# Kernel optimization log

Hardware: AMD Instinct MI355X
Metric: run time of the kernel (lower is better)

## Reference

```python
import jax, jax.numpy as jnp
import numpy as np

EPS = 1e-6


def _rmsnorm(x, w):
    var = jnp.mean(x * x, axis=-1, keepdims=True)
    return x * jax.lax.rsqrt(var + EPS) * w


def _rotate_half(x):
    h = x.shape[-1] // 2
    return jnp.concatenate([-x[..., h:], x[..., :h]], axis=-1)


def setup_inputs() -> dict:
    key = jax.random.key(0)
    B, T, H = 2, 2048, 2048
    nh, nkv, d = 16, 8, 128
    max_pos = 4096
    ks = jax.random.split(key, 6)
    s = 0.02
    x = jax.random.normal(ks[0], (B, T, H), jnp.float32)
    # real RoPE tables (Qwen3 uses rope_theta=1e6)
    inv_freq = 1.0 / (1e6 ** (np.arange(0, d, 2, dtype=np.float64) / d))
    freqs = np.outer(np.arange(max_pos), inv_freq)
    emb = np.concatenate([freqs, freqs], axis=-1)
    cos = jnp.asarray(np.cos(emb), jnp.float32)
    sin = jnp.asarray(np.sin(emb), jnp.float32)
    position_ids = jnp.broadcast_to(jnp.arange(T, dtype=jnp.int32)[None, :], (B, T))
    Wq = jax.random.normal(ks[1], (nh * d, H), jnp.float32) * s
    Wk = jax.random.normal(ks[2], (nkv * d, H), jnp.float32) * s
    Wv = jax.random.normal(ks[3], (nkv * d, H), jnp.float32) * s
    Wo = jax.random.normal(ks[4], (H, nh * d), jnp.float32) * s
    q_norm_w = jnp.ones((d,), jnp.float32)
    k_norm_w = jnp.ones((d,), jnp.float32)
    return {"x": x, "cos": cos, "sin": sin, "position_ids": position_ids,
            "Wq": Wq, "Wk": Wk, "Wv": Wv, "Wo": Wo,
            "q_norm_w": q_norm_w, "k_norm_w": k_norm_w}


def reference(x, cos, sin, position_ids, Wq, Wk, Wv, Wo, q_norm_w, k_norm_w):
    B, T, H = x.shape
    d = q_norm_w.shape[0]
    nh = Wq.shape[0] // d
    nkv = Wk.shape[0] // d
    groups = nh // nkv

    # QKV projections (F.linear: x @ W.T)
    q = jnp.einsum('bth,oh->bto', x, Wq).reshape(B, T, nh, d).transpose(0, 2, 1, 3)   # [B,nh,T,d]
    k = jnp.einsum('bth,oh->bto', x, Wk).reshape(B, T, nkv, d).transpose(0, 2, 1, 3)  # [B,nkv,T,d]
    v = jnp.einsum('bth,oh->bto', x, Wv).reshape(B, T, nkv, d).transpose(0, 2, 1, 3)

    # per-head RMSNorm on q and k
    q = _rmsnorm(q, q_norm_w)
    k = _rmsnorm(k, k_norm_w)

    # RoPE
    cos_b = cos[position_ids][:, None, :, :]  # [B,1,T,d]
    sin_b = sin[position_ids][:, None, :, :]
    q = q * cos_b + _rotate_half(q) * sin_b
    k = k * cos_b + _rotate_half(k) * sin_b

    # GQA expand (repeat_interleave along head dim)
    if groups > 1:
        k = jnp.repeat(k, groups, axis=1)
        v = jnp.repeat(v, groups, axis=1)

    # causal SDPA
    scale = 1.0 / jnp.sqrt(jnp.asarray(d, x.dtype))
    scores = jnp.einsum('bhqd,bhkd->bhqk', q, k) * scale  # [B,nh,T,T]
    causal = jnp.tril(jnp.ones((T, T), bool))
    scores = jnp.where(causal[None, None], scores, jnp.asarray(-jnp.inf, scores.dtype))
    probs = jax.nn.softmax(scores, axis=-1)
    attn = jnp.einsum('bhqk,bhkd->bhqd', probs, v)  # [B,nh,T,d]

    attn = attn.transpose(0, 2, 1, 3).reshape(B, T, nh * d)
    return jnp.einsum('bto,ho->bth', attn, Wo)
```

## Files before the change

### kernel.cpp

```cpp
#include <hip/hip_runtime.h>
#include <stdint.h>
#include <stddef.h>

typedef unsigned short u16;
typedef __attribute__((ext_vector_type(4))) unsigned short u16x4;
typedef __attribute__((ext_vector_type(8))) short bf16x8;
typedef __attribute__((ext_vector_type(4))) float f32x4;
typedef __attribute__((ext_vector_type(16))) float f32x16;

#define B_   2
#define T_   2048
#define NH   16
#define NKV  8
#define HD   128

#define QSCALE 0.1275174457f

__device__ __forceinline__ u16 f2bf(float f) {
  union { float f; uint32_t u; } v; v.f = f;
  uint32_t u = v.u;
  u += 0x7FFFu + ((u >> 16) & 1u);
  return (u16)(u >> 16);
}
__device__ __forceinline__ float bf2f(u16 h) {
  union { uint32_t u; float f; } v; v.u = ((uint32_t)h) << 16;
  return v.f;
}
__device__ __forceinline__ uint32_t cvt_pk_bf16(float lo, float hi) {
  uint32_t r;
  asm("v_cvt_pk_bf16_f32 %0, %1, %2" : "=v"(r) : "v"(lo), "v"(hi));
  return r;
}
__device__ __forceinline__ float fexp2(float x) {
  float r;
  asm("v_exp_f32 %0, %1" : "=v"(r) : "v"(x));
  return r;
}

__device__ __forceinline__ void gload_lds16(const void* g, void* l) {
  __builtin_amdgcn_global_load_lds(
      (__attribute__((address_space(1))) void*)g,
      (__attribute__((address_space(3))) void*)l, 16, 0, 0);
}

__global__ __launch_bounds__(256) void cvt_all(const float* __restrict__ x,
                                               const float* __restrict__ Wq,
                                               const float* __restrict__ Wk,
                                               const float* __restrict__ Wv,
                                               const float* __restrict__ Wo,
                                               u16* __restrict__ ws0) {
  const int blk = blockIdx.x;
  const float* src; u16* dst; int lb;
  if (blk < 8192)       { src = x;  dst = ws0;              lb = blk; }
  else if (blk < 12288) { src = Wq; dst = ws0 +  8388608;   lb = blk - 8192; }
  else if (blk < 14336) { src = Wk; dst = ws0 + 12582912;   lb = blk - 12288; }
  else if (blk < 16384) { src = Wv; dst = ws0 + 14680064;   lb = blk - 14336; }
  else                  { src = Wo; dst = ws0 + 16777216;   lb = blk - 16384; }
  const int i = lb * 256 + threadIdx.x;
  float4 v = reinterpret_cast<const float4*>(src)[i];
  u16x4 o;
  o.x = f2bf(v.x); o.y = f2bf(v.y); o.z = f2bf(v.z); o.w = f2bf(v.w);
  reinterpret_cast<u16x4*>(dst)[i] = o;
}

template<int BM, int BN, int STORE>
__global__ __launch_bounds__(512, 2) void gemm2(const u16* __restrict__ A,
                                                const u16* __restrict__ Bm,
                                                void* __restrict__ C0,
                                                void* __restrict__ C1,
                                                void* __restrict__ C2,
                                                int M, int N, int K) {
  constexpr int FM  = BM / 32;
  constexpr int FN  = BN / 64;
  constexpr int ASZ = BM * 64;
  constexpr int BSZ = BN * 64;
  __shared__ u16 lds[2 * (ASZ + BSZ)];

  const int tid  = threadIdx.x;
  const int lane = tid & 63;
  const int wid  = tid >> 6;
  const int lr   = lane & 15;
  const int lg   = lane >> 4;
  const int wm0 = (wid >> 2) * (BM / 2);
  const int wn0 = (wid & 3) * (BN / 4);

  const int s  = ((blockIdx.x & 7) << 5) | (blockIdx.x >> 3);
  const int nx = N / BN;
  const int m0 = (s / nx) * BM;
  const int n0 = (s % nx) * BN;

  f32x4 acc[FM][FN];
#pragma unroll
  for (int i = 0; i < FM; ++i)
#pragma unroll
    for (int j = 0; j < FN; ++j) acc[i][j] = (f32x4){0.f, 0.f, 0.f, 0.f};

  auto stage = [&](int kt, int p) {
    const int k0 = kt << 6;
    u16* Ab = lds + p * (ASZ + BSZ);
    u16* Bb = Ab + ASZ;
#pragma unroll
    for (int it = 0; it < BM / 64; ++it) {
      const int CI = it * 512 + tid;
      const int row = CI >> 3, c = CI & 7;
      gload_lds16(A + (size_t)(m0 + row) * K + k0 + ((c ^ (row & 7)) << 3),
                  (char*)Ab + (size_t)CI * 16);
    }
#pragma unroll
    for (int it = 0; it < BN / 64; ++it) {
      const int CI = it * 512 + tid;
      const int row = CI >> 3, c = CI & 7;
      gload_lds16(Bm + (size_t)(n0 + row) * K + k0 + ((c ^ (row & 7)) << 3),
                  (char*)Bb + (size_t)CI * 16);
    }
  };

  const int nk = K >> 6;
  stage(0, 0);
  __syncthreads();
  int cur = 0;
  for (int kt = 0; kt < nk; ++kt) {
    if (kt + 1 < nk) stage(kt + 1, cur ^ 1);
    const u16* Ab = lds + cur * (ASZ + BSZ);
    const u16* Bb = Ab + ASZ;
#pragma unroll
    for (int kk = 0; kk < 2; ++kk) {
      bf16x8 af[FM], bfr[FN];
#pragma unroll
      for (int mt = 0; mt < FM; ++mt) {
        const int ar = wm0 + mt * 16 + lr;
        af[mt] = *reinterpret_cast<const bf16x8*>(
            (const char*)Ab + ar * 128 + ((kk * 64 + lg * 16) ^ ((ar & 7) << 4)));
      }
#pragma unroll
      for (int nt = 0; nt < FN; ++nt) {
        const int br = wn0 + nt * 16 + lr;
        bfr[nt] = *reinterpret_cast<const bf16x8*>(
            (const char*)Bb + br * 128 + ((kk * 64 + lg * 16) ^ ((br & 7) << 4)));
      }
      __builtin_amdgcn_s_setprio(1);
#pragma unroll
      for (int mt = 0; mt < FM; ++mt)
#pragma unroll
        for (int nt = 0; nt < FN; ++nt)
          acc[mt][nt] = __builtin_amdgcn_mfma_f32_16x16x32_bf16(
              af[mt], bfr[nt], acc[mt][nt], 0, 0, 0);
      __builtin_amdgcn_s_setprio(0);
    }
    __syncthreads();
    cur ^= 1;
  }

  if (STORE == 3) {
    u16* Qd = (u16*)C0; u16* Kd = (u16*)C1; u16* Vd = (u16*)C2;
    if (n0 < 2048) {
#pragma unroll
      for (int mt = 0; mt < FM; ++mt) {
        const int row = m0 + wm0 + mt * 16 + lg * 4;
#pragma unroll
        for (int nt = 0; nt < FN; ++nt) {
          const int col = n0 + wn0 + nt * 16 + lr;
#pragma unroll
          for (int r = 0; r < 4; ++r)
            Qd[(size_t)(row + r) * 2048 + col] = f2bf(acc[mt][nt][r]);
        }
      }
    } else if (n0 < 3072) {
#pragma unroll
      for (int mt = 0; mt < FM; ++mt) {
        const int row = m0 + wm0 + mt * 16 + lg * 4;
#pragma unroll
        for (int nt = 0; nt < FN; ++nt) {
          const int col = n0 + wn0 + nt * 16 + lr - 2048;
#pragma unroll
          for (int r = 0; r < 4; ++r)
            Kd[(size_t)(row + r) * 1024 + col] = f2bf(acc[mt][nt][r]);
        }
      }
    } else {
#pragma unroll
      for (int mt = 0; mt < FM; ++mt) {
        const int row = m0 + wm0 + mt * 16 + lg * 4;
        const int b = row >> 11;
        const int t = row & (T_ - 1);
#pragma unroll
        for (int nt = 0; nt < FN; ++nt) {
          const int vc = n0 + wn0 + nt * 16 + lr - 3072;
          u16x4 v;
          v.x = f2bf(acc[mt][nt][0]); v.y = f2bf(acc[mt][nt][1]);
          v.z = f2bf(acc[mt][nt][2]); v.w = f2bf(acc[mt][nt][3]);
          *reinterpret_cast<u16x4*>(Vd + ((size_t)(b * 1024 + vc)) * T_ + t) = v;
        }
      }
    }
  } else {
    float* C = (float*)C0;
#pragma unroll
    for (int mt = 0; mt < FM; ++mt) {
      const int row = m0 + wm0 + mt * 16 + lg * 4;
#pragma unroll
      for (int nt = 0; nt < FN; ++nt) {
        const int col = n0 + wn0 + nt * 16 + lr;
#pragma unroll
        for (int r = 0; r < 4; ++r)
          C[(size_t)(row + r) * N + col] = acc[mt][nt][r];
      }
    }
  }
}

__global__ __launch_bounds__(256) void rms_rope(u16* __restrict__ Q, u16* __restrict__ Kb,
                                                const float* __restrict__ cosT,
                                                const float* __restrict__ sinT,
                                                const int* __restrict__ pos,
                                                const float* __restrict__ qw,
                                                const float* __restrict__ kw) {
  const int wave = blockIdx.x * 4 + (threadIdx.x >> 6);
  const int lane = threadIdx.x & 63;
  const int bt = wave & (B_ * T_ - 1);
  const int hh = wave >> 12;
  u16* ptr;
  const float* w;
  float post;
  if (hh < NH) { ptr = Q + (size_t)bt * (NH * HD) + hh * HD; w = qw; post = QSCALE; }
  else         { ptr = Kb + (size_t)bt * (NKV * HD) + (hh - NH) * HD; w = kw; post = 1.0f; }
  const int p = pos[bt];

  float e0 = bf2f(ptr[lane]);
  float e1 = bf2f(ptr[lane + 64]);
  float ss = e0 * e0 + e1 * e1;
#pragma unroll
  for (int off = 1; off < 64; off <<= 1) ss += __shfl_xor(ss, off, 64);
  const float r = rsqrtf(ss * (1.0f / 128.0f) + 1e-6f) * post;
  const float n0 = e0 * r * w[lane];
  const float n1 = e1 * r * w[lane + 64];
  const float c0 = cosT[(size_t)p * HD + lane], c1 = cosT[(size_t)p * HD + lane + 64];
  const float s0 = sinT[(size_t)p * HD + lane], s1 = sinT[(size_t)p * HD + lane + 64];
  ptr[lane]      = f2bf(n0 * c0 - n1 * s0);
  ptr[lane + 64] = f2bf(n1 * c1 + n0 * s1);
}

__global__ __launch_bounds__(256, 2) void flash_attn5(const u16* __restrict__ Qw,
                                                      const u16* __restrict__ Kw,
                                                      const u16* __restrict__ VTw,
                                                      u16* __restrict__ Ow) {
  __shared__ __align__(16) char smem[65536];

  const int tid  = threadIdx.x;
  const int lane = tid & 63;
  const int wid  = tid >> 6;
  const int rl   = lane & 31;
  const int hi   = lane >> 5;
  const int blk  = blockIdx.x;
  const int qtr = blk >> 5;
  const int qt  = (blk < 256) ? (15 - qtr) : (qtr - 8);
  const int bh  = blk & 31;
  const int b   = bh >> 4, h = bh & 15, kvh = h >> 1;
  const int q0w = qt * 128 + wid * 32;
  const int qg  = q0w + rl;
  const int kswz = (rl & 15) << 4;
  const int vswz = (rl & 7) << 4;

  bf16x8 qf[8];
  {
    const u16* qp = Qw + ((size_t)(b * T_) + qg) * (NH * HD) + h * HD + hi * 8;
#pragma unroll
    for (int kd = 0; kd < 8; ++kd) qf[kd] = *reinterpret_cast<const bf16x8*>(qp + kd * 16);
  }

  f32x16 ot[4];
#pragma unroll
  for (int dt = 0; dt < 4; ++dt)
#pragma unroll
    for (int r = 0; r < 16; ++r) ot[dt][r] = 0.f;
  float m = -1e30f, lsum = 0.f;

  auto stageKV = [&](int kt, int p) {
    char* Kb = smem + p * 32768;
    char* Vb = Kb + 16384;
    {
      const int row = tid >> 4, ch = tid & 15;
#pragma unroll
      for (int it = 0; it < 4; ++it) {
        const int rr = it * 16 + row;
        const int scol = ((ch * 16) ^ ((rr & 15) << 4)) >> 1;
        gload_lds16(Kw + ((size_t)(b * T_) + kt * 64 + rr) * (NKV * HD) + kvh * HD + scol,
                    Kb + (it * 256 + tid) * 16);
      }
    }
    {
      const int row = tid >> 3, ch = tid & 7;
#pragma unroll
      for (int it = 0; it < 4; ++it) {
        const int rr = it * 32 + row;
        const int scol = ((ch * 16) ^ ((rr & 7) << 4)) >> 1;
        gload_lds16(VTw + ((size_t)((b * NKV + kvh) * HD) + rr) * T_ + kt * 64 + scol,
                    Vb + (it * 256 + tid) * 16);
      }
    }
  };

  const int nkt = 2 * qt + 2;
  stageKV(0, 0);
  __syncthreads();
  for (int kt = 0; kt < nkt; ++kt) {
    const int cur = kt & 1;
    if (kt + 1 < nkt) stageKV(kt + 1, cur ^ 1);

    if (64 * kt <= q0w + 31) {
      const u16* Kb = (const u16*)(smem + cur * 32768);
      const u16* Vb = (const u16*)(smem + cur * 32768 + 16384);

      f32x16 s0, s1;
#pragma unroll
      for (int r = 0; r < 16; ++r) { s0[r] = 0.f; s1[r] = 0.f; }
      __builtin_amdgcn_s_setprio(1);
#pragma unroll
      for (int kd = 0; kd < 8; ++kd) {
        const int cb = (kd * 32 + hi * 16) ^ kswz;
        const bf16x8 k0 = *reinterpret_cast<const bf16x8*>((const char*)Kb + rl * 256 + cb);
        const bf16x8 k1 = *reinterpret_cast<const bf16x8*>((const char*)Kb + (32 + rl) * 256 + cb);
        s0 = __builtin_amdgcn_mfma_f32_32x32x16_bf16(k0, qf[kd], s0, 0, 0, 0);
        s1 = __builtin_amdgcn_mfma_f32_32x32x16_bf16(k1, qf[kd], s1, 0, 0, 0);
      }
      __builtin_amdgcn_s_setprio(0);

      const int kv0 = kt * 64;
      const bool maskT = (kv0 + 63 > q0w);
      float rm = -1e30f;
      if (maskT) {
#pragma unroll
        for (int r = 0; r < 16; ++r) {
          const int cr = (r & 3) + 8 * (r >> 2) + 4 * hi;
          float a = s0[r], c = s1[r];
          if (kv0 + cr > qg)      a = -1e30f;
          if (kv0 + 32 + cr > qg) c = -1e30f;
          s0[r] = a; s1[r] = c;
          rm = fmaxf(rm, fmaxf(a, c));
        }
      } else {
#pragma unroll
        for (int r = 0; r < 16; ++r) rm = fmaxf(rm, fmaxf(s0[r], s1[r]));
      }
      rm = fmaxf(rm, __shfl_xor(rm, 32));

      if (!__all(rm <= m + 8.0f)) {
        const float mn = fmaxf(m, rm);
        const float al = fexp2(m - mn);
        lsum *= al;
#pragma unroll
        for (int dt = 0; dt < 4; ++dt)
#pragma unroll
          for (int r = 0; r < 16; ++r) ot[dt][r] *= al;
        m = mn;
      }
      float rs = 0.f;
#pragma unroll
      for (int r = 0; r < 16; ++r) {
        const float p0 = fexp2(s0[r] - m);
        const float p1 = fexp2(s1[r] - m);
        s0[r] = p0; s1[r] = p1;
        rs += p0 + p1;
      }
      rs += __shfl_xor(rs, 32);
      lsum += rs;

      bf16x8 pf[2][2];
#pragma unroll
      for (int ks = 0; ks < 2; ++ks) {
        {
          uint32_t X0 = cvt_pk_bf16(s0[8 * ks + 0], s0[8 * ks + 1]);
          uint32_t X1 = cvt_pk_bf16(s0[8 * ks + 2], s0[8 * ks + 3]);
          uint32_t Y0 = cvt_pk_bf16(s0[8 * ks + 4], s0[8 * ks + 5]);
          uint32_t Y1 = cvt_pk_bf16(s0[8 * ks + 6], s0[8 * ks + 7]);
          asm volatile("v_permlane32_swap_b32 %0, %1" : "+v"(X0), "+v"(Y0));
          asm volatile("v_permlane32_swap_b32 %0, %1" : "+v"(X1), "+v"(Y1));
          union { uint32_t w[4]; bf16x8 v; } u;
          u.w[0] = X0; u.w[1] = X1; u.w[2] = Y0; u.w[3] = Y1;
          pf[0][ks] = u.v;
        }
        {
          uint32_t X0 = cvt_pk_bf16(s1[8 * ks + 0], s1[8 * ks + 1]);
          uint32_t X1 = cvt_pk_bf16(s1[8 * ks + 2], s1[8 * ks + 3]);
          uint32_t Y0 = cvt_pk_bf16(s1[8 * ks + 4], s1[8 * ks + 5]);
          uint32_t Y1 = cvt_pk_bf16(s1[8 * ks + 6], s1[8 * ks + 7]);
          asm volatile("v_permlane32_swap_b32 %0, %1" : "+v"(X0), "+v"(Y0));
          asm volatile("v_permlane32_swap_b32 %0, %1" : "+v"(X1), "+v"(Y1));
          union { uint32_t w[4]; bf16x8 v; } u;
          u.w[0] = X0; u.w[1] = X1; u.w[2] = Y0; u.w[3] = Y1;
          pf[1][ks] = u.v;
        }
      }

      __builtin_amdgcn_s_setprio(1);
#pragma unroll
      for (int dt = 0; dt < 4; ++dt) {
        const int rv = dt * 32 + rl;
#pragma unroll
        for (int kvc = 0; kvc < 2; ++kvc)
#pragma unroll
          for (int ks = 0; ks < 2; ++ks) {
            const int cb = (kvc * 64 + ks * 32 + hi * 16) ^ ((rv & 7) << 4);
            const bf16x8 vf = *reinterpret_cast<const bf16x8*>((const char*)Vb + rv * 128 + cb);
            ot[dt] = __builtin_amdgcn_mfma_f32_32x32x16_bf16(vf, pf[kvc][ks], ot[dt], 0, 0, 0);
          }
      }
      __builtin_amdgcn_s_setprio(0);
    }
    __syncthreads();
  }

  const float inv = 1.0f / lsum;
  u16* ep = (u16*)smem + wid * (32 * 136);
#pragma unroll
  for (int dt = 0; dt < 4; ++dt)
#pragma unroll
    for (int r = 0; r < 16; ++r) {
      const int d = dt * 32 + (r & 3) + 8 * (r >> 2) + 4 * hi;
      ep[rl * 136 + d] = f2bf(ot[dt][r] * inv);
    }
  const int dh = hi * 64;
  const u16* srcp = (u16*)smem + wid * (32 * 136) + rl * 136 + dh;
  u16* gdst = Ow + ((size_t)(b * T_) + q0w + rl) * (NH * HD) + h * HD + dh;
#pragma unroll
  for (int c2 = 0; c2 < 8; ++c2)
    *reinterpret_cast<bf16x8*>(gdst + c2 * 8) =
        *reinterpret_cast<const bf16x8*>(srcp + c2 * 8);
}

extern "C" void kernel_launch(void* const* d_in, const int* in_sizes, int n_in,
                              void* d_out, int out_size, void* d_ws, size_t ws_size,
                              hipStream_t stream) {
  (void)in_sizes; (void)n_in; (void)out_size; (void)ws_size;
  const float* x    = (const float*)d_in[0];
  const float* cosT = (const float*)d_in[1];
  const float* sinT = (const float*)d_in[2];
  const int*   pos  = (const int*)d_in[3];
  const float* Wq   = (const float*)d_in[4];
  const float* Wk   = (const float*)d_in[5];
  const float* Wv   = (const float*)d_in[6];
  const float* Wo   = (const float*)d_in[7];
  const float* qw   = (const float*)d_in[8];
  const float* kw   = (const float*)d_in[9];
  float* out = (float*)d_out;

  char* ws = (char*)d_ws;
  u16* xb   = (u16*)(ws + 0);
  u16* Wqb  = (u16*)(ws + 16777216);
  u16* Wob  = (u16*)(ws + 33554432);
  u16* Qws  = (u16*)(ws + 41943040);
  u16* Kws  = (u16*)(ws + 58720256);
  u16* VTws = (u16*)(ws + 67108864);
  u16* Aws  = (u16*)(ws + 75497472);

  cvt_all<<<20480, 256, 0, stream>>>(x, Wq, Wk, Wv, Wo, (u16*)ws);

  gemm2<256, 256, 3><<<256, 512, 0, stream>>>(xb, Wqb, Qws, Kws, VTws,
                                              4096, 4096, 2048);

  rms_rope<<<24576, 256, 0, stream>>>(Qws, Kws, cosT, sinT, pos, qw, kw);

  flash_attn5<<<512, 256, 0, stream>>>(Qws, Kws, VTws, Aws);

  gemm2<128, 256, 2><<<256, 512, 0, stream>>>(Aws, Wob, out, nullptr, nullptr,
                                              4096, 2048, 2048);
}
```

Before: 191.5 us.

## Add finely pipelined QKV GEMM kernel with interleaved half-tile staging

Adds a dedicated 256x256 QKV projection GEMM that splits each K-step into four MFMA phases. Each phase issues half-tile global-to-LDS loads for upcoming steps, with explicit vmcnt waits and barriers, so loads overlap compute more finely than the old double-buffered loop. It also uses a block-index swizzle for tile scheduling. The cost is more barriers and hand-tuned wait counts, which are fragile if the load counts change.

```diff
diff --git a/kernel.cpp b/kernel.cpp
--- a/kernel.cpp
+++ b/kernel.cpp
@@ -42,6 +42,11 @@
       (__attribute__((address_space(1))) void*)g,
       (__attribute__((address_space(3))) void*)l, 16, 0, 0);
 }
+
+#define WAITVM(N) do { asm volatile("s_waitcnt vmcnt(" #N ")" ::: "memory"); \
+                       __builtin_amdgcn_sched_barrier(0); } while (0)
+#define BAR()     do { __builtin_amdgcn_s_barrier(); \
+                       __builtin_amdgcn_sched_barrier(0); } while (0)
 
 __global__ __launch_bounds__(256) void cvt_all(const float* __restrict__ x,
                                                const float* __restrict__ Wq,
@@ -63,6 +68,195 @@
   reinterpret_cast<u16x4*>(dst)[i] = o;
 }
 
+__global__ __launch_bounds__(512, 2) void gemm3(const u16* __restrict__ A,
+                                                const u16* __restrict__ Bm,
+                                                void* __restrict__ C0,
+                                                void* __restrict__ C1,
+                                                void* __restrict__ C2,
+                                                int M, int N, int K) {
+  constexpr int BM = 256, BN = 256;
+  constexpr int ASZ = BM * 64;
+  constexpr int BSZ = BN * 64;
+  constexpr int RSZ = ASZ + BSZ;
+  __shared__ u16 lds[2 * RSZ];
+
+  const int tid  = threadIdx.x;
+  const int lane = tid & 63;
+  const int wid  = tid >> 6;
+  const int lr   = lane & 15;
+  const int lg   = lane >> 4;
+  const int wm0 = (wid >> 2) * 128;
+  const int wn0 = (wid & 3) * 64;
+
+  const int s  = ((blockIdx.x & 7) << 5) | (blockIdx.x >> 3);
+  const int nx = N / BN;
+  const int m0 = (s / nx) * BM;
+  const int n0 = (s % nx) * BN;
+
+  f32x4 acc[8][4];
+#pragma unroll
+  for (int i = 0; i < 8; ++i)
+#pragma unroll
+    for (int j = 0; j < 4; ++j) acc[i][j] = (f32x4){0.f, 0.f, 0.f, 0.f};
+
+  auto stageA = [&](int kt, int xh) {
+    u16* Ab = lds + (kt & 1) * RSZ;
+    const int k0 = kt << 6;
+#pragma unroll
+    for (int j = 0; j < 2; ++j) {
+      const int rowblk = j * 128 + xh * 64;
+      const int row = rowblk + (tid >> 3), c = tid & 7;
+      gload_lds16(A + (size_t)(m0 + row) * K + k0 + ((c ^ (row & 7)) << 3),
+                  (char*)Ab + ((size_t)rowblk * 8 + tid) * 16);
+    }
+  };
+  auto stageB = [&](int kt, int nh) {
+    u16* Bb = lds + (kt & 1) * RSZ + ASZ;
+    const int k0 = kt << 6;
+#pragma unroll
+    for (int j = 0; j < 2; ++j) {
+      const int blk2 = j * 2 + (tid >> 8);
+      const int row = blk2 * 64 + nh * 32 + ((tid & 255) >> 3);
+      const int c = tid & 7;
+      gload_lds16(Bm + (size_t)(n0 + row) * K + k0 + ((c ^ (row & 7)) << 3),
+                  (char*)Bb + ((size_t)row * 8 + c) * 16);
+    }
+  };
+
+  const int nk = K >> 6;
+
+  stageA(0, 0); stageB(0, 0); stageA(0, 1); stageB(0, 1);
+  stageA(1, 0); stageB(1, 0);
+  WAITVM(8);
+  BAR();
+
+  bf16x8 af[4][2], bf[2][2];
+
+#define LOAD_A(Ab, mh)                                                        \
+  _Pragma("unroll")                                                           \
+  for (int mt2 = 0; mt2 < 4; ++mt2)                                           \
+    _Pragma("unroll")                                                         \
+    for (int kk = 0; kk < 2; ++kk) {                                          \
+      const int ar = wm0 + ((mh) * 4 + mt2) * 16 + lr;                        \
+      af[mt2][kk] = *reinterpret_cast<const bf16x8*>(                         \
+          (const char*)(Ab) + ar * 128 + ((kk * 64 + lg * 16) ^ ((ar & 7) << 4))); \
+    }
+#define LOAD_B(Bb, nh)                                                        \
+  _Pragma("unroll")                                                           \
+  for (int nt2 = 0; nt2 < 2; ++nt2)                                           \
+    _Pragma("unroll")                                                         \
+    for (int kk = 0; kk < 2; ++kk) {                                          \
+      const int br = wn0 + ((nh) * 2 + nt2) * 16 + lr;                        \
+      bf[nt2][kk] = *reinterpret_cast<const bf16x8*>(                         \
+          (const char*)(Bb) + br * 128 + ((kk * 64 + lg * 16) ^ ((br & 7) << 4))); \
+    }
+#define MFMA_PHASE(mh, nh)                                                    \
+  __builtin_amdgcn_s_setprio(1);                                              \
+  _Pragma("unroll")                                                           \
+  for (int mt2 = 0; mt2 < 4; ++mt2)                                           \
+    _Pragma("unroll")                                                         \
+    for (int nt2 = 0; nt2 < 2; ++nt2)                                         \
+      _Pragma("unroll")                                                       \
+      for (int kk = 0; kk < 2; ++kk)                                          \
+        acc[(mh) * 4 + mt2][(nh) * 2 + nt2] =                                 \
+            __builtin_amdgcn_mfma_f32_16x16x32_bf16(                          \
+                af[mt2][kk], bf[nt2][kk], acc[(mh) * 4 + mt2][(nh) * 2 + nt2],\
+                0, 0, 0);                                                     \
+  __builtin_amdgcn_s_setprio(0);
+
+  for (int t = 0; t <= nk - 3; ++t) {
+    const u16* Ab = lds + (t & 1) * RSZ;
+    const u16* Bb = Ab + ASZ;
+    LOAD_A(Ab, 0); LOAD_B(Bb, 0);
+    stageA(t + 1, 1);
+    WAITVM(6); BAR();
+    MFMA_PHASE(0, 0);
+    BAR();
+    LOAD_B(Bb, 1);
+    stageB(t + 1, 1);
+    WAITVM(10); BAR();
+    MFMA_PHASE(0, 1);
+    BAR();
+    LOAD_A(Ab, 1); LOAD_B(Bb, 0);
+    stageA(t + 2, 0);
+    WAITVM(10); BAR();
+    MFMA_PHASE(1, 0);
+    BAR();
+    LOAD_B(Bb, 1);
+    stageB(t + 2, 0);
+    WAITVM(8); BAR();
+    MFMA_PHASE(1, 1);
+    BAR();
+  }
+
+  stageA(nk - 1, 1); stageB(nk - 1, 1);
+  WAITVM(0);
+  BAR();
+
+#pragma unroll
+  for (int e = 0; e < 2; ++e) {
+    const int t = nk - 2 + e;
+    const u16* Ab = lds + (t & 1) * RSZ;
+    const u16* Bb = Ab + ASZ;
+#pragma unroll
+    for (int mh = 0; mh < 2; ++mh) {
+      LOAD_A(Ab, mh);
+#pragma unroll
+      for (int nh = 0; nh < 2; ++nh) {
+        LOAD_B(Bb, nh);
+        MFMA_PHASE(mh, nh);
+      }
+    }
+  }
+
+  {
+    u16* Qd = (u16*)C0; u16* Kd = (u16*)C1; u16* Vd = (u16*)C2;
+    if (n0 < 2048) {
+#pragma unroll
+      for (int mt = 0; mt < 8; ++mt) {
+        const int row = m0 + wm0 + mt * 16 + lg * 4;
+#pragma unroll
+        for (int nt = 0; nt < 4; ++nt) {
+          const int col = n0 + wn0 + nt * 16 + lr;
+#pragma unroll
+          for (int r = 0; r < 4; ++r)
+            Qd[(size_t)(row + r) * 2048 + col] = f2bf(acc[mt][nt][r]);
+        }
+      }
+    } else if (n0 < 3072) {
+#pragma unroll
+      for (int mt = 0; mt < 8; ++mt) {
+        const int row = m0 + wm0 + mt * 16 + lg * 4;
+#pragma unroll
+        for (int nt = 0; nt < 4; ++nt) {
+          const int col = n0 + wn0 + nt * 16 + lr - 2048;
+#pragma unroll
+          for (int r = 0; r < 4; ++r)
+            Kd[(size_t)(row + r) * 1024 + col] = f2bf(acc[mt][nt][r]);
+        }
+      }
+    } else {
+#pragma unroll
+      for (int mt = 0; mt < 8; ++mt) {
+        const int row = m0 + wm0 + mt * 16 + lg * 4;
+        const int b = row >> 11;
+        const int t = row & (T_ - 1);
+#pragma unroll
+        for (int nt = 0; nt < 4; ++nt) {
+          const int vc = n0 + wn0 + nt * 16 + lr - 3072;
+          u16x4 v;
+          v.x = f2bf(acc[mt][nt][0]); v.y = f2bf(acc[mt][nt][1]);
+          v.z = f2bf(acc[mt][nt][2]); v.w = f2bf(acc[mt][nt][3]);
+          *reinterpret_cast<u16x4*>(Vd + ((size_t)(b * 1024 + vc)) * T_ + t) = v;
+        }
+      }
+    }
+  }
+#undef LOAD_A
+#undef LOAD_B
+#undef MFMA_PHASE
+}
+
 template<int BM, int BN, int STORE>
 __global__ __launch_bounds__(512, 2) void gemm2(const u16* __restrict__ A,
                                                 const u16* __restrict__ Bm,
@@ -151,49 +345,7 @@
     cur ^= 1;
   }
 
-  if (STORE == 3) {
-    u16* Qd = (u16*)C0; u16* Kd = (u16*)C1; u16* Vd = (u16*)C2;
-    if (n0 < 2048) {
-#pragma unroll
-      for (int mt = 0; mt < FM; ++mt) {
-        const int row = m0 + wm0 + mt * 16 + lg * 4;
-#pragma unroll
-        for (int nt = 0; nt < FN; ++nt) {
-          const int col = n0 + wn0 + nt * 16 + lr;
-#pragma unroll
-          for (int r = 0; r < 4; ++r)
-            Qd[(size_t)(row + r) * 2048 + col] = f2bf(acc[mt][nt][r]);
-        }
-      }
-    } else if (n0 < 3072) {
-#pragma unroll
-      for (int mt = 0; mt < FM; ++mt) {
-        const int row = m0 + wm0 + mt * 16 + lg * 4;
-#pragma unroll
-        for (int nt = 0; nt < FN; ++nt) {
-          const int col = n0 + wn0 + nt * 16 + lr - 2048;
-#pragma unroll
-          for (int r = 0; r < 4; ++r)
-            Kd[(size_t)(row + r) * 1024 + col] = f2bf(acc[mt][nt][r]);
-        }
-      }
-    } else {
-#pragma unroll
-      for (int mt = 0; mt < FM; ++mt) {
-        const int row = m0 + wm0 + mt * 16 + lg * 4;
-        const int b = row >> 11;
-        const int t = row & (T_ - 1);
-#pragma unroll
-        for (int nt = 0; nt < FN; ++nt) {
-          const int vc = n0 + wn0 + nt * 16 + lr - 3072;
-          u16x4 v;
-          v.x = f2bf(acc[mt][nt][0]); v.y = f2bf(acc[mt][nt][1]);
-          v.z = f2bf(acc[mt][nt][2]); v.w = f2bf(acc[mt][nt][3]);
-          *reinterpret_cast<u16x4*>(Vd + ((size_t)(b * 1024 + vc)) * T_ + t) = v;
-        }
-      }
-    }
-  } else {
+  if (STORE == 2) {
     float* C = (float*)C0;
 #pragma unroll
     for (int mt = 0; mt < FM; ++mt) {
@@ -259,7 +411,6 @@
   const int q0w = qt * 128 + wid * 32;
   const int qg  = q0w + rl;
   const int kswz = (rl & 15) << 4;
-  const int vswz = (rl & 7) << 4;
 
   bf16x8 qf[8];
   {
@@ -455,8 +606,7 @@
 
   cvt_all<<<20480, 256, 0, stream>>>(x, Wq, Wk, Wv, Wo, (u16*)ws);
 
-  gemm2<256, 256, 3><<<256, 512, 0, stream>>>(xb, Wqb, Qws, Kws, VTws,
-                                              4096, 4096, 2048);
+  gemm3<<<256, 512, 0, stream>>>(xb, Wqb, Qws, Kws, VTws, 4096, 4096, 2048);
 
   rms_rope<<<24576, 256, 0, stream>>>(Qws, Kws, cosT, sinT, pos, qw, kw);
 
```

Result: no change. 193.2 us (+0.9%).
